# Kernel tuning notes

Hardware: AMD Instinct MI355X
Metric: run time of the kernel (lower is better)

Reference implementation:

```python
import jax, jax.numpy as jnp
import numpy as np

B, T, D, H = 256, 256, 64, 512  # batch, seq_len, input_dim, hidden_dim


def setup_inputs() -> dict:
    key = jax.random.key(0)
    ks = jax.random.split(key, 12)
    scale = 0.05
    inp = {"x": jax.random.normal(ks[0], (B, T, D), dtype=jnp.float32)}
    in_dims = [D, H, H]
    for i in range(3):
        inp[f"Wx{i}"] = jax.random.normal(ks[1 + 3 * i], (in_dims[i], H), dtype=jnp.float32) * scale
        inp[f"Wh{i}"] = jax.random.normal(ks[2 + 3 * i], (H, H), dtype=jnp.float32) * scale
        inp[f"b{i}"] = jnp.zeros((H,), dtype=jnp.float32)
    inp["Wf"] = jax.random.normal(ks[10], (H, 1), dtype=jnp.float32) * scale
    inp["bf"] = jnp.zeros((1,), dtype=jnp.float32)
    return inp


def _rnn_seq(x, Wx, Wh, b):
    """SimpleRNN with return_sequences=True. x: [B,T,Din] -> [B,T,H].
    Keras eval mode: dropout inactive. h_t = tanh(x_t Wx + h_{t-1} Wh + b)."""
    # Precompute input projection for all steps (one big GEMM).
    xp = jnp.einsum('btd,dh->bth', x, Wx) + b  # [B,T,H]

    def step(h, xt):
        h2 = jnp.tanh(xt + h @ Wh)
        return h2, h2

    h0 = jnp.zeros((x.shape[0], Wh.shape[0]), dtype=x.dtype)
    _, ys = jax.lax.scan(step, h0, jnp.swapaxes(xp, 0, 1))  # ys: [T,B,H]
    return jnp.swapaxes(ys, 0, 1)


def _rnn_last(x, Wx, Wh, b):
    """SimpleRNN with return_sequences=False. x: [B,T,Din] -> [B,H] (final state)."""
    xp = jnp.einsum('btd,dh->bth', x, Wx) + b

    def step(h, xt):
        h2 = jnp.tanh(xt + h @ Wh)
        return h2, None

    h0 = jnp.zeros((x.shape[0], Wh.shape[0]), dtype=x.dtype)
    hT, _ = jax.lax.scan(step, h0, jnp.swapaxes(xp, 0, 1))
    return hT


def reference(x, Wx0, Wh0, b0, Wx1, Wh1, b1, Wx2, Wh2, b2, Wf, bf):
    h = _rnn_seq(x, Wx0, Wh0, b0)   # [B,T,H]
    h = _rnn_seq(h, Wx1, Wh1, b1)   # [B,T,H]
    h = _rnn_last(h, Wx2, Wh2, b2)  # [B,H]
    return h @ Wf + bf              # [B,1]
```

## Files before the change

kernel.cpp:

```cpp
#include <hip/hip_runtime.h>


typedef unsigned short u16;
typedef unsigned int   u32;

typedef __attribute__((ext_vector_type(8))) short short8;
typedef __attribute__((ext_vector_type(4))) float f32x4;
typedef __attribute__((ext_vector_type(4))) int   i32x4;

#define N_B 256
#define N_T 256
#define N_D 64
#define N_H 512
#define LAY 3
#define BG  8
#define CGS 8
#define ROWS 32
#define WCOL 64
#define CNT_TGT 8
#define HSK_TGT 24
#define CPAD 16
#define CNT_LINES (LAY * BG * N_T)
#define CNT_U32   ((CNT_LINES + 2 * BG) * CPAD)
#define SPIN_LIM (1u << 22)

__device__ __forceinline__ u16 f2bf(float f) {
  union { float f; u32 u; } v; v.f = f;
  u32 u = v.u;
  u += 0x7fffu + ((u >> 16) & 1u);
  return (u16)(u >> 16);
}
__device__ __forceinline__ float bf2f(u16 h) {
  union { u32 u; float f; } v; v.u = ((u32)h) << 16;
  return v.f;
}
__device__ __forceinline__ short8 ld8(const u16* p) { return *(const short8*)p; }
__device__ __forceinline__ short8 cvt8(const float* p) {
  short8 r;
#pragma unroll
  for (int j = 0; j < 8; ++j) r[j] = (short)f2bf(p[j]);
  return r;
}
__device__ __forceinline__ short8 as_s8(i32x4 v) {
  union { i32x4 i; short8 s; } u; u.i = v; return u.s;
}
__device__ __forceinline__ float fast_tanh(float x) {
  float xc = fminf(fmaxf(x, -9.f), 9.f);
  float e  = __builtin_amdgcn_exp2f(xc * 2.8853900817779268f);
  return 1.f - 2.f * __builtin_amdgcn_rcpf(e + 1.f);
}
__device__ __forceinline__ u32 rmw_read(u32* p) {
  u32 v, z = 0;
  asm volatile("global_atomic_add %0, %1, %2, off sc0\n\ts_waitcnt vmcnt(0)"
               : "=v"(v) : "v"(p), "v"(z) : "memory");
  return v;
}
__device__ __forceinline__ void poll_cnt(u32* cp, u32 target, bool fast, bool* dead) {
  u32 it = 0;
  for (;;) {
    u32 v = fast ? rmw_read(cp)
                 : __hip_atomic_load(cp, __ATOMIC_RELAXED, __HIP_MEMORY_SCOPE_AGENT);
    if (v >= target) return;
    if (it >= 2) __builtin_amdgcn_s_sleep(1);
    if (++it > SPIN_LIM) { *dead = true; return; }
  }
}
__device__ __forceinline__ void lds_set(volatile u32* f, u32 v) {
  __hip_atomic_store((u32*)f, v, __ATOMIC_RELEASE, __HIP_MEMORY_SCOPE_WORKGROUP);
}
__device__ __forceinline__ void lds_wait(volatile u32* f, u32 want, bool* dead) {
  u32 it = 0;
  while (__hip_atomic_load((u32*)f, __ATOMIC_ACQUIRE, __HIP_MEMORY_SCOPE_WORKGROUP) != want) {
    if (++it > SPIN_LIM) { *dead = true; return; }
  }
}

__device__ __forceinline__ void load16_async_fast(const u16* p, i32x4 f[16]) {
  asm volatile(
      "global_load_dwordx4 %0, %16, off sc0\n\t"
      "global_load_dwordx4 %1, %16, off offset:64 sc0\n\t"
      "global_load_dwordx4 %2, %16, off offset:128 sc0\n\t"
      "global_load_dwordx4 %3, %16, off offset:192 sc0\n\t"
      "global_load_dwordx4 %4, %16, off offset:256 sc0\n\t"
      "global_load_dwordx4 %5, %16, off offset:320 sc0\n\t"
      "global_load_dwordx4 %6, %16, off offset:384 sc0\n\t"
      "global_load_dwordx4 %7, %16, off offset:448 sc0\n\t"
      "global_load_dwordx4 %8, %16, off offset:512 sc0\n\t"
      "global_load_dwordx4 %9, %16, off offset:576 sc0\n\t"
      "global_load_dwordx4 %10, %16, off offset:640 sc0\n\t"
      "global_load_dwordx4 %11, %16, off offset:704 sc0\n\t"
      "global_load_dwordx4 %12, %16, off offset:768 sc0\n\t"
      "global_load_dwordx4 %13, %16, off offset:832 sc0\n\t"
      "global_load_dwordx4 %14, %16, off offset:896 sc0\n\t"
      "global_load_dwordx4 %15, %16, off offset:960 sc0"
      : "=&v"(f[0]), "=&v"(f[1]), "=&v"(f[2]), "=&v"(f[3]),
        "=&v"(f[4]), "=&v"(f[5]), "=&v"(f[6]), "=&v"(f[7]),
        "=&v"(f[8]), "=&v"(f[9]), "=&v"(f[10]), "=&v"(f[11]),
        "=&v"(f[12]), "=&v"(f[13]), "=&v"(f[14]), "=&v"(f[15])
      : "v"(p) : "memory");
}
__device__ __forceinline__ void load16_async_slow(const u16* p, i32x4 f[16]) {
  asm volatile(
      "global_load_dwordx4 %0, %16, off sc0 sc1\n\t"
      "global_load_dwordx4 %1, %16, off offset:64 sc0 sc1\n\t"
      "global_load_dwordx4 %2, %16, off offset:128 sc0 sc1\n\t"
      "global_load_dwordx4 %3, %16, off offset:192 sc0 sc1\n\t"
      "global_load_dwordx4 %4, %16, off offset:256 sc0 sc1\n\t"
      "global_load_dwordx4 %5, %16, off offset:320 sc0 sc1\n\t"
      "global_load_dwordx4 %6, %16, off offset:384 sc0 sc1\n\t"
      "global_load_dwordx4 %7, %16, off offset:448 sc0 sc1\n\t"
      "global_load_dwordx4 %8, %16, off offset:512 sc0 sc1\n\t"
      "global_load_dwordx4 %9, %16, off offset:576 sc0 sc1\n\t"
      "global_load_dwordx4 %10, %16, off offset:640 sc0 sc1\n\t"
      "global_load_dwordx4 %11, %16, off offset:704 sc0 sc1\n\t"
      "global_load_dwordx4 %12, %16, off offset:768 sc0 sc1\n\t"
      "global_load_dwordx4 %13, %16, off offset:832 sc0 sc1\n\t"
      "global_load_dwordx4 %14, %16, off offset:896 sc0 sc1\n\t"
      "global_load_dwordx4 %15, %16, off offset:960 sc0 sc1"
      : "=&v"(f[0]), "=&v"(f[1]), "=&v"(f[2]), "=&v"(f[3]),
        "=&v"(f[4]), "=&v"(f[5]), "=&v"(f[6]), "=&v"(f[7]),
        "=&v"(f[8]), "=&v"(f[9]), "=&v"(f[10]), "=&v"(f[11]),
        "=&v"(f[12]), "=&v"(f[13]), "=&v"(f[14]), "=&v"(f[15])
      : "v"(p) : "memory");
}

#define MFMA16(a, b, c) __builtin_amdgcn_mfma_f32_16x16x32_bf16((a), (b), (c), 0, 0, 0)

#define STEPK(kt, N)                                                        \
  do {                                                                      \
    asm volatile("s_waitcnt vmcnt(" #N ")" : "+v"(fr[kt]) :: "memory");     \
    short8 a_ = as_s8(fr[kt]);                                              \
    acc[0] = MFMA16(a_, wf[kt][0], acc[0]);                                 \
    acc[1] = MFMA16(a_, wf[kt][1], acc[1]);                                 \
    acc[2] = MFMA16(a_, wf[kt][2], acc[2]);                                 \
    acc[3] = MFMA16(a_, wf[kt][3], acc[3]);                                 \
  } while (0)
#define K16_PIPE()                                                          \
  STEPK(0, 15); STEPK(1, 14); STEPK(2, 13); STEPK(3, 12);                   \
  STEPK(4, 11); STEPK(5, 10); STEPK(6, 9);  STEPK(7, 8);                    \
  STEPK(8, 7);  STEPK(9, 6);  STEPK(10, 5); STEPK(11, 4);                   \
  STEPK(12, 3); STEPK(13, 2); STEPK(14, 1); STEPK(15, 0)

__global__ __launch_bounds__(256, 1)
void rnn_pipe(const float* __restrict__ x,
              const float* __restrict__ Wx0, const float* __restrict__ Wh0, const float* __restrict__ b0,
              const float* __restrict__ Wx1, const float* __restrict__ Wh1, const float* __restrict__ b1,
              const float* __restrict__ Wx2, const float* __restrict__ Wh2, const float* __restrict__ b2,
              u16* __restrict__ seq0, u16* __restrict__ seq1, u16* __restrict__ seq2,
              u32* __restrict__ cnt) {
  const int b    = blockIdx.x & 7;
  const int rst  = blockIdx.x >> 3;
  const int layer = rst >> 3;
  const int j    = rst & 7;
  const int tid  = threadIdx.x;
  const int lane = tid & 63;
  const int w    = tid >> 6;
  const int quad = lane >> 4;
  const int l16  = lane & 15;
  const int half = w & 1;
  const bool is_rec = (w < 2);

  const float *Wx, *Wh, *bias; const u16 *in_seq = nullptr; u16 *out_seq;
  if (layer == 0)      { Wx = Wx0; Wh = Wh0; bias = b0; out_seq = seq0; }
  else if (layer == 1) { Wx = Wx1; Wh = Wh1; bias = b1; in_seq = seq0; out_seq = seq1; }
  else                 { Wx = Wx2; Wh = Wh2; bias = b2; in_seq = seq1; out_seq = seq2; }
  const int kin = (layer == 0) ? N_D : N_H;
  u32* cnt_own  = cnt + (size_t)(layer * BG + b) * N_T * CPAD;
  u32* cnt_prev = (layer > 0) ? cnt + (size_t)((layer - 1) * BG + b) * N_T * CPAD : nullptr;
  u32* hsk_arr  = cnt + (size_t)(CNT_LINES + b) * CPAD;
  u32* hsk_msk  = cnt + (size_t)(CNT_LINES + BG + b) * CPAD;

  __shared__ u16   WhT[WCOL][N_H];
  __shared__ u16   WxT[WCOL][N_H];
  __shared__ float Cbuf[2][ROWS][WCOL + 1];
  __shared__ u32   fastsh;
  __shared__ u32   sflags[6];

  u32 xcc;
  asm volatile("s_getreg_b32 %0, hwreg(HW_REG_XCC_ID)" : "=s"(xcc));
  if (tid == 0) {
    __hip_atomic_fetch_or(hsk_msk, 1u << (xcc & 7), __ATOMIC_RELAXED,
                          __HIP_MEMORY_SCOPE_AGENT);
    asm volatile("s_waitcnt vmcnt(0)" ::: "memory");
    __hip_atomic_fetch_add(hsk_arr, 1u, __ATOMIC_RELAXED, __HIP_MEMORY_SCOPE_AGENT);
  }
  if (tid < 6) sflags[tid] = 0;

  for (int e = tid; e < WCOL * N_H; e += 256) {
    int n = e & 63, k = e >> 6;
    WhT[n][(k + 8 * n) & (N_H - 1)] = f2bf(Wh[k * N_H + j * WCOL + n]);
  }
  for (int e = tid; e < WCOL * kin; e += 256) {
    int n = e & 63, k = e >> 6;
    WxT[n][(k + 8 * n) & (kin - 1)] = f2bf(Wx[k * N_H + j * WCOL + n]);
  }
  float bv[4];
#pragma unroll
  for (int n = 0; n < 4; ++n) bv[n] = bias[j * WCOL + n * 16 + l16];

  if (tid == 0) {
    bool f = false;
    u32 it = 0;
    while (rmw_read(hsk_arr) < (u32)HSK_TGT) {
      __builtin_amdgcn_s_sleep(1);
      if (++it > SPIN_LIM) break;
    }
    if (it <= SPIN_LIM) {
      u32 m = rmw_read(hsk_msk);
      f = (m != 0u) && ((m & (m - 1u)) == 0u);
    }
    fastsh = f ? 1u : 0u;
  }
  __syncthreads();
  const bool fast = (fastsh == 1u);

  short8 wf[16][4];
  if (is_rec) {
#pragma unroll
    for (int kt = 0; kt < 16; ++kt)
#pragma unroll
      for (int n = 0; n < 4; ++n) {
        int nl = n * 16 + l16;
        wf[kt][n] = ld8(&WhT[nl][(kt * 32 + quad * 8 + 8 * nl) & (N_H - 1)]);
      }
  } else if (layer == 0) {
#pragma unroll
    for (int n = 0; n < 4; ++n) {
      int nl = n * 16 + l16;
      wf[0][n] = ld8(&WxT[nl][(quad * 8 + 8 * nl) & (N_D - 1)]);
      wf[1][n] = ld8(&WxT[nl][(32 + quad * 8 + 8 * nl) & (N_D - 1)]);
    }
  } else {
#pragma unroll
    for (int kt = 0; kt < 16; ++kt)
#pragma unroll
      for (int n = 0; n < 4; ++n) {
        int nl = n * 16 + l16;
        wf[kt][n] = ld8(&WxT[nl][(kt * 32 + quad * 8 + 8 * nl) & (N_H - 1)]);
      }
  }

  const int arow = b * ROWS + half * 16 + l16;
  bool dead = false;

  for (int t = 0; t < N_T; ++t) {
    const int par = t & 1;
    f32x4 acc[4] = {{0.f,0.f,0.f,0.f},{0.f,0.f,0.f,0.f},{0.f,0.f,0.f,0.f},{0.f,0.f,0.f,0.f}};

    if (!is_rec) {
      if (layer == 0) {
        const float* xp = x + ((size_t)arow * N_T + t) * N_D + quad * 8;
        short8 f0 = cvt8(xp), f1 = cvt8(xp + 32);
#pragma unroll
        for (int n = 0; n < 4; ++n) {
          acc[n] = MFMA16(f0, wf[0][n], acc[n]);
          acc[n] = MFMA16(f1, wf[1][n], acc[n]);
        }
      } else {
        if (half == 0) {
          if (lane == 0) {
            if (!dead) poll_cnt(cnt_prev + (size_t)t * CPAD, CNT_TGT, fast, &dead);
            lds_set(&sflags[2 + par], (u32)(t + 1));
          }
        } else {
          if (lane == 0 && !dead) lds_wait(&sflags[2 + par], (u32)(t + 1), &dead);
        }
        const u16* sp = in_seq + ((size_t)t * N_B + arow) * N_H + quad * 8;
        i32x4 fr[16];
        if (fast) load16_async_fast(sp, fr);
        else      load16_async_slow(sp, fr);
        K16_PIPE();
      }
      int rb = half * 16 + quad * 4;
#pragma unroll
      for (int n = 0; n < 4; ++n)
#pragma unroll
        for (int r = 0; r < 4; ++r)
          Cbuf[par][rb + r][n * 16 + l16] = acc[n][r];
    } else {
      if (t > 0) {
        if (half == 0) {
          if (lane == 0) {
            if (!dead) poll_cnt(cnt_own + (size_t)(t - 1) * CPAD, CNT_TGT, fast, &dead);
            lds_set(&sflags[par], (u32)t);
          }
        } else {
          if (lane == 0 && !dead) lds_wait(&sflags[par], (u32)t, &dead);
        }
        const u16* ap = out_seq + ((size_t)(t - 1) * N_B + arow) * N_H + quad * 8;
        i32x4 fr[16];
        if (fast) load16_async_fast(ap, fr);
        else      load16_async_slow(ap, fr);
        K16_PIPE();
      }
    }

    __syncthreads();

    if (is_rec) {
      int rb = half * 16 + quad * 4;
      u32 hv[4][4];
#pragma unroll
      for (int n = 0; n < 4; ++n)
#pragma unroll
        for (int r = 0; r < 4; ++r)
          hv[n][r] = (u32)f2bf(fast_tanh(acc[n][r] + Cbuf[par][rb + r][n * 16 + l16] + bv[n]));
      u16* hdst = out_seq + ((size_t)t * N_B + b * ROWS + half * 16 + quad * 4) * N_H
                  + j * WCOL + l16;
      if (fast) {
        asm volatile(
            "global_store_short %0, %1, off sc0\n\t"
            "global_store_short %0, %2, off offset:1024 sc0\n\t"
            "global_store_short %0, %3, off offset:2048 sc0\n\t"
            "global_store_short %0, %4, off offset:3072 sc0\n\t"
            "global_store_short %0, %5, off offset:32 sc0\n\t"
            "global_store_short %0, %6, off offset:1056 sc0\n\t"
            "global_store_short %0, %7, off offset:2080 sc0\n\t"
            "global_store_short %0, %8, off offset:3104 sc0\n\t"
            "global_store_short %0, %9, off offset:64 sc0\n\t"
            "global_store_short %0, %10, off offset:1088 sc0\n\t"
            "global_store_short %0, %11, off offset:2112 sc0\n\t"
            "global_store_short %0, %12, off offset:3136 sc0\n\t"
            "global_store_short %0, %13, off offset:96 sc0\n\t"
            "global_store_short %0, %14, off offset:1120 sc0\n\t"
            "global_store_short %0, %15, off offset:2144 sc0\n\t"
            "global_store_short %0, %16, off offset:3168 sc0"
            :: "v"(hdst),
               "v"(hv[0][0]), "v"(hv[0][1]), "v"(hv[0][2]), "v"(hv[0][3]),
               "v"(hv[1][0]), "v"(hv[1][1]), "v"(hv[1][2]), "v"(hv[1][3]),
               "v"(hv[2][0]), "v"(hv[2][1]), "v"(hv[2][2]), "v"(hv[2][3]),
               "v"(hv[3][0]), "v"(hv[3][1]), "v"(hv[3][2]), "v"(hv[3][3])
            : "memory");
      } else {
        asm volatile(
            "global_store_short %0, %1, off sc0 sc1\n\t"
            "global_store_short %0, %2, off offset:1024 sc0 sc1\n\t"
            "global_store_short %0, %3, off offset:2048 sc0 sc1\n\t"
            "global_store_short %0, %4, off offset:3072 sc0 sc1\n\t"
            "global_store_short %0, %5, off offset:32 sc0 sc1\n\t"
            "global_store_short %0, %6, off offset:1056 sc0 sc1\n\t"
            "global_store_short %0, %7, off offset:2080 sc0 sc1\n\t"
            "global_store_short %0, %8, off offset:3104 sc0 sc1\n\t"
            "global_store_short %0, %9, off offset:64 sc0 sc1\n\t"
            "global_store_short %0, %10, off offset:1088 sc0 sc1\n\t"
            "global_store_short %0, %11, off offset:2112 sc0 sc1\n\t"
            "global_store_short %0, %12, off offset:3136 sc0 sc1\n\t"
            "global_store_short %0, %13, off offset:96 sc0 sc1\n\t"
            "global_store_short %0, %14, off offset:1120 sc0 sc1\n\t"
            "global_store_short %0, %15, off offset:2144 sc0 sc1\n\t"
            "global_store_short %0, %16, off offset:3168 sc0 sc1"
            :: "v"(hdst),
               "v"(hv[0][0]), "v"(hv[0][1]), "v"(hv[0][2]), "v"(hv[0][3]),
               "v"(hv[1][0]), "v"(hv[1][1]), "v"(hv[1][2]), "v"(hv[1][3]),
               "v"(hv[2][0]), "v"(hv[2][1]), "v"(hv[2][2]), "v"(hv[2][3]),
               "v"(hv[3][0]), "v"(hv[3][1]), "v"(hv[3][2]), "v"(hv[3][3])
            : "memory");
      }
      asm volatile("s_waitcnt vmcnt(0)" ::: "memory");
      if (half == 1) {
        if (lane == 0) lds_set(&sflags[4 + par], (u32)(t + 1));
      } else {
        if (lane == 0) {
          if (!dead) lds_wait(&sflags[4 + par], (u32)(t + 1), &dead);
          u32* cp = cnt_own + (size_t)t * CPAD;
          if (fast) {
            u32 one = 1u;
            asm volatile("global_atomic_add %0, %1, off" :: "v"(cp), "v"(one) : "memory");
          } else {
            __hip_atomic_fetch_add(cp, 1u, __ATOMIC_RELAXED, __HIP_MEMORY_SCOPE_AGENT);
          }
        }
      }
    }
  }
}

__global__ void head_kernel(const u16* __restrict__ seq2, const float* __restrict__ Wf,
                            const float* __restrict__ bf, float* __restrict__ out) {
  int b    = blockIdx.x;
  int lane = threadIdx.x;
  const u16* hrow = seq2 + ((size_t)(N_T - 1) * N_B + b) * N_H;
  float s = 0.f;
#pragma unroll
  for (int r = 0; r < N_H / 64; ++r) {
    int idx = lane * 8 + r;
    s += bf2f(hrow[idx]) * Wf[idx];
  }
#pragma unroll
  for (int off = 32; off > 0; off >>= 1) s += __shfl_down(s, off);
  if (lane == 0) out[b] = s + bf[0];
}

extern "C" void kernel_launch(void* const* d_in, const int* in_sizes, int n_in,
                              void* d_out, int out_size, void* d_ws, size_t ws_size,
                              hipStream_t stream) {
  const float* x   = (const float*)d_in[0];
  const float* Wx0 = (const float*)d_in[1];
  const float* Wh0 = (const float*)d_in[2];
  const float* b0  = (const float*)d_in[3];
  const float* Wx1 = (const float*)d_in[4];
  const float* Wh1 = (const float*)d_in[5];
  const float* b1  = (const float*)d_in[6];
  const float* Wx2 = (const float*)d_in[7];
  const float* Wh2 = (const float*)d_in[8];
  const float* b2  = (const float*)d_in[9];
  const float* Wf  = (const float*)d_in[10];
  const float* bf  = (const float*)d_in[11];
  float* out = (float*)d_out;

  const size_t SEQ_BYTES = (size_t)N_T * N_B * N_H * sizeof(u16);
  if (ws_size < 3 * SEQ_BYTES + (size_t)CNT_U32 * sizeof(u32)) return;

  char* ws  = (char*)d_ws;
  u16* seq0 = (u16*)(ws);
  u16* seq1 = (u16*)(ws + SEQ_BYTES);
  u16* seq2 = (u16*)(ws + 2 * SEQ_BYTES);
  u32* cnt  = (u32*)(ws + 3 * SEQ_BYTES);

  (void)hipMemsetAsync(cnt, 0, (size_t)CNT_U32 * sizeof(u32), stream);

  rnn_pipe<<<LAY * BG * CGS, 256, 0, stream>>>(x, Wx0, Wh0, b0, Wx1, Wh1, b1,
                                               Wx2, Wh2, b2, seq0, seq1, seq2,
                                               cnt);
  head_kernel<<<N_B, 64, 0, stream>>>(seq2, Wf, bf, out);
}
```

Baseline: 1.086 ms.

## Assign batch-group roles by XCC so each group's workgroups share one XCC

Replaces the fixed blockIdx-to-(batch group, layer, column) mapping with a dynamic assignment. All 192 workgroups first publish their XCC id and meet at a global barrier, then each computes a deterministic role so that the 24 workgroups of a batch group land on the same XCC where possible. Groups fully on one XCC can use the fast same-XCC synchronisation path, cutting cross-die coherence traffic in the per-timestep handshakes. It adds a grid-wide barrier at startup and falls back to the static mapping if the barrier times out.

```diff
diff --git a/kernel.cpp b/kernel.cpp
--- a/kernel.cpp
+++ b/kernel.cpp
@@ -3,6 +3,7 @@
 
 typedef unsigned short u16;
 typedef unsigned int   u32;
+typedef unsigned long long u64;
 
 typedef __attribute__((ext_vector_type(8))) short short8;
 typedef __attribute__((ext_vector_type(4))) float f32x4;
@@ -17,11 +18,13 @@
 #define CGS 8
 #define ROWS 32
 #define WCOL 64
+#define NWG (LAY * BG * CGS)
 #define CNT_TGT 8
-#define HSK_TGT 24
 #define CPAD 16
 #define CNT_LINES (LAY * BG * N_T)
-#define CNT_U32   ((CNT_LINES + 2 * BG) * CPAD)
+#define XBASE ((CNT_LINES + 2 * BG) * CPAD)
+#define XCCS  (XBASE + CPAD)
+#define CNT_U32 (XCCS + NWG)
 #define SPIN_LIM (1u << 22)
 
 __device__ __forceinline__ u16 f2bf(float f) {
@@ -148,10 +151,6 @@
               const float* __restrict__ Wx2, const float* __restrict__ Wh2, const float* __restrict__ b2,
               u16* __restrict__ seq0, u16* __restrict__ seq1, u16* __restrict__ seq2,
               u32* __restrict__ cnt) {
-  const int b    = blockIdx.x & 7;
-  const int rst  = blockIdx.x >> 3;
-  const int layer = rst >> 3;
-  const int j    = rst & 7;
   const int tid  = threadIdx.x;
   const int lane = tid & 63;
   const int w    = tid >> 6;
@@ -160,6 +159,74 @@
   const int half = w & 1;
   const bool is_rec = (w < 2);
 
+  __shared__ u16   WhT[WCOL][N_H];
+  __shared__ u16   WxT[WCOL][N_H];
+  __shared__ float Cbuf[2][ROWS][WCOL + 1];
+  __shared__ u32   sflags[6];
+  __shared__ u32   sx[NWG];
+  __shared__ u32   sbar;
+
+  u32* arrive = cnt + XBASE;
+  u32* xccs   = cnt + XCCS;
+
+  u32 xcc;
+  asm volatile("s_getreg_b32 %0, hwreg(HW_REG_XCC_ID)" : "=s"(xcc));
+  if (tid == 0) {
+    u32* xe = xccs + blockIdx.x;
+    u32 xv = xcc & 7u;
+    asm volatile("global_store_dword %0, %1, off sc0 sc1\n\ts_waitcnt vmcnt(0)"
+                 :: "v"(xe), "v"(xv) : "memory");
+    __hip_atomic_fetch_add(arrive, 1u, __ATOMIC_RELAXED, __HIP_MEMORY_SCOPE_AGENT);
+    u32 it = 0; u32 bd = 0;
+    while (rmw_read(arrive) < (u32)NWG) {
+      __builtin_amdgcn_s_sleep(1);
+      if (++it > SPIN_LIM) { bd = 1; break; }
+    }
+    sbar = bd;
+  }
+  if (tid < 6) sflags[tid] = 0;
+  __syncthreads();
+  const bool bar_dead = (sbar != 0);
+  if (!bar_dead && tid < NWG) sx[tid] = rmw_read(xccs + tid) & 7u;
+  __syncthreads();
+
+  int bg, layer, j; bool fast;
+  if (bar_dead) {
+    bg = blockIdx.x & 7;
+    int rst = blockIdx.x >> 3;
+    layer = rst >> 3; j = rst & 7;
+    fast = false;
+  } else {
+    u64 c64 = 0;
+    int myrid = -1, mypend = -1, pends = 0;
+    for (int i = 0; i < NWG; ++i) {
+      u32 xv = sx[i];
+      u32 c = (u32)((c64 >> (8u * xv)) & 0xffu);
+      if (c < 24u) {
+        if (i == (int)blockIdx.x) myrid = (int)(xv * 24u + c);
+        c64 += (1ull << (8u * xv));
+      } else {
+        if (i == (int)blockIdx.x) mypend = pends;
+        ++pends;
+      }
+    }
+    if (myrid < 0) {
+      int p = 0;
+      for (int xb = 0; xb < 8; ++xb) {
+        u32 c = (u32)((c64 >> (8u * xb)) & 0xffu);
+        for (u32 s = c; s < 24u; ++s) {
+          if (p == mypend) myrid = xb * 24 + (int)s;
+          ++p;
+        }
+      }
+    }
+    bg = myrid / 24;
+    int slot = myrid % 24;
+    layer = slot >> 3; j = slot & 7;
+    fast = (((c64 >> (8u * (u32)bg)) & 0xffu) >= 24u);
+  }
+  const int b = bg;
+
   const float *Wx, *Wh, *bias; const u16 *in_seq = nullptr; u16 *out_seq;
   if (layer == 0)      { Wx = Wx0; Wh = Wh0; bias = b0; out_seq = seq0; }
   else if (layer == 1) { Wx = Wx1; Wh = Wh1; bias = b1; in_seq = seq0; out_seq = seq1; }
@@ -167,24 +234,6 @@
   const int kin = (layer == 0) ? N_D : N_H;
   u32* cnt_own  = cnt + (size_t)(layer * BG + b) * N_T * CPAD;
   u32* cnt_prev = (layer > 0) ? cnt + (size_t)((layer - 1) * BG + b) * N_T * CPAD : nullptr;
-  u32* hsk_arr  = cnt + (size_t)(CNT_LINES + b) * CPAD;
-  u32* hsk_msk  = cnt + (size_t)(CNT_LINES + BG + b) * CPAD;
-
-  __shared__ u16   WhT[WCOL][N_H];
-  __shared__ u16   WxT[WCOL][N_H];
-  __shared__ float Cbuf[2][ROWS][WCOL + 1];
-  __shared__ u32   fastsh;
-  __shared__ u32   sflags[6];
-
-  u32 xcc;
-  asm volatile("s_getreg_b32 %0, hwreg(HW_REG_XCC_ID)" : "=s"(xcc));
-  if (tid == 0) {
-    __hip_atomic_fetch_or(hsk_msk, 1u << (xcc & 7), __ATOMIC_RELAXED,
-                          __HIP_MEMORY_SCOPE_AGENT);
-    asm volatile("s_waitcnt vmcnt(0)" ::: "memory");
-    __hip_atomic_fetch_add(hsk_arr, 1u, __ATOMIC_RELAXED, __HIP_MEMORY_SCOPE_AGENT);
-  }
-  if (tid < 6) sflags[tid] = 0;
 
   for (int e = tid; e < WCOL * N_H; e += 256) {
     int n = e & 63, k = e >> 6;
@@ -197,22 +246,7 @@
   float bv[4];
 #pragma unroll
   for (int n = 0; n < 4; ++n) bv[n] = bias[j * WCOL + n * 16 + l16];
-
-  if (tid == 0) {
-    bool f = false;
-    u32 it = 0;
-    while (rmw_read(hsk_arr) < (u32)HSK_TGT) {
-      __builtin_amdgcn_s_sleep(1);
-      if (++it > SPIN_LIM) break;
-    }
-    if (it <= SPIN_LIM) {
-      u32 m = rmw_read(hsk_msk);
-      f = (m != 0u) && ((m & (m - 1u)) == 0u);
-    }
-    fastsh = f ? 1u : 0u;
-  }
   __syncthreads();
-  const bool fast = (fastsh == 1u);
 
   short8 wf[16][4];
   if (is_rec) {
```

New measurement: 1.079 ms. About the same (-0.6%).
